# Kernel optimization log

Hardware: AMD Instinct MI355X
Metric: run time of the kernel (lower is better)

Reference implementation:

```python
import jax, jax.numpy as jnp
import numpy as np

N_NODES = 50000
N_EDGES = 600000
D_IN = 128
D_HID = 128
NUM_LAYERS = 4


def setup_inputs() -> dict:
    key = jax.random.key(0)
    ks = jax.random.split(key, 8)
    x = jax.random.normal(ks[0], (N_NODES, D_IN), dtype=jnp.float32)
    edge_index = jax.random.randint(ks[1], (2, N_EDGES), 0, N_NODES, dtype=jnp.int32)
    s = 0.05
    # first_conv: lin_rel (weight+bias) applied to aggregated neighbors, lin_root (no bias) applied to x
    W1 = jax.random.normal(ks[2], (D_IN, D_HID), dtype=jnp.float32) * s
    b1 = jnp.zeros((D_HID,), dtype=jnp.float32)
    R1 = jax.random.normal(ks[3], (D_IN, D_HID), dtype=jnp.float32) * s
    # shared conv used for layers 2..NUM_LAYERS
    W2 = jax.random.normal(ks[4], (D_HID, D_HID), dtype=jnp.float32) * s
    b2 = jnp.zeros((D_HID,), dtype=jnp.float32)
    R2 = jax.random.normal(ks[5], (D_HID, D_HID), dtype=jnp.float32) * s
    return {"x": x, "edge_index": edge_index, "W1": W1, "b1": b1, "R1": R1,
            "W2": W2, "b2": b2, "R2": R2}


def _graph_conv(x, src, dst, W, b, R, num_nodes):
    # gather source features, scatter-max into destinations (PyG GraphConv, aggr='max')
    agg = jax.ops.segment_max(x[src], dst, num_segments=num_nodes)  # [N, d]
    agg = jnp.where(jnp.isneginf(agg), 0.0, agg)  # isolated nodes -> 0 (PyG fill)
    return agg @ W + b + x @ R  # lin_rel(agg) + lin_root(x)


def reference(x, edge_index, W1, b1, R1, W2, b2, R2):
    src, dst = edge_index[0], edge_index[1]
    n = x.shape[0]
    h = jax.nn.relu(_graph_conv(x, src, dst, W1, b1, R1, n))
    for _ in range(NUM_LAYERS - 1):  # shared weights, per original module
        h = jax.nn.relu(_graph_conv(h, src, dst, W2, b2, R2, n))
    return h
```

## Files before the change

### kernel.cpp

```cpp
#include <hip/hip_runtime.h>
#include <math.h>

static constexpr int NNODES = 50000;
static constexpr int NEDGES = 600000;
static constexpr int D = 128;

typedef __attribute__((ext_vector_type(8))) short short8;
typedef __attribute__((ext_vector_type(4))) float f32x4;

static __device__ inline unsigned short f2bf_rne(float f) {
  unsigned u = __float_as_uint(f);
  unsigned r = (u + 0x7FFFu + ((u >> 16) & 1u)) >> 16;
  return (unsigned short)r;
}
static __device__ inline float bf2f(unsigned short s) {
  return __uint_as_float(((unsigned)s) << 16);
}


__global__ void count_kernel(const int* __restrict__ dst, int* __restrict__ cnt, int nE) {
  int i = blockIdx.x * blockDim.x + threadIdx.x;
  if (i < nE) atomicAdd(&cnt[dst[i]], 1);
}

__global__ void scan_kernel(const int* __restrict__ cnt, int* __restrict__ rs, int n) {
  __shared__ int wsum[16];
  __shared__ int s_carry;
  if (threadIdx.x == 0) s_carry = 0;
  __syncthreads();
  const int wid = threadIdx.x >> 6;
  const int lane = threadIdx.x & 63;
  for (int base = 0; base < n; base += 1024) {
    int i = base + (int)threadIdx.x;
    int v = (i < n) ? cnt[i] : 0;
    int incl = v;
#pragma unroll
    for (int off = 1; off < 64; off <<= 1) {
      int t = __shfl_up(incl, off);
      if (lane >= off) incl += t;
    }
    if (lane == 63) wsum[wid] = incl;
    __syncthreads();
    int woff = s_carry;
    for (int w = 0; w < wid; ++w) woff += wsum[w];
    if (i < n) rs[i] = woff + incl - v;
    __syncthreads();
    if (threadIdx.x == 1023) s_carry = woff + incl;
    __syncthreads();
  }
  if (threadIdx.x == 0) rs[n] = s_carry;
}

__global__ void fill_kernel(const int* __restrict__ src, const int* __restrict__ dst,
                            int* __restrict__ cursor, int* __restrict__ csr, int nE) {
  int i = blockIdx.x * blockDim.x + threadIdx.x;
  if (i < nE) {
    int d = dst[i];
    int p = atomicAdd(&cursor[d], 1);
    csr[p] = src[i];
  }
}

__global__ __launch_bounds__(256) void agg_kernel(const float* __restrict__ x,
    const int* __restrict__ rs, const int* __restrict__ csr,
    float* __restrict__ agg, int n) {
  int gw = (int)((blockIdx.x * blockDim.x + threadIdx.x) >> 6);
  int lane = threadIdx.x & 63;
  if (gw >= n) return;
  int beg = rs[gw], end = rs[gw + 1];
  const float2* xx = (const float2*)x;
  float2 acc;
  acc.x = -INFINITY; acc.y = -INFINITY;
  int j = beg;
  for (; j + 4 <= end; j += 4) {
    int s0 = csr[j], s1 = csr[j + 1], s2 = csr[j + 2], s3 = csr[j + 3];
    float2 v0 = xx[s0 * 64 + lane];
    float2 v1 = xx[s1 * 64 + lane];
    float2 v2 = xx[s2 * 64 + lane];
    float2 v3 = xx[s3 * 64 + lane];
    acc.x = fmaxf(fmaxf(fmaxf(v0.x, v1.x), fmaxf(v2.x, v3.x)), acc.x);
    acc.y = fmaxf(fmaxf(fmaxf(v0.y, v1.y), fmaxf(v2.y, v3.y)), acc.y);
  }
  for (; j < end; ++j) {
    int s = csr[j];
    float2 v = xx[s * 64 + lane];
    acc.x = fmaxf(acc.x, v.x);
    acc.y = fmaxf(acc.y, v.y);
  }
  if (beg == end) { acc.x = 0.f; acc.y = 0.f; }
  ((float2*)agg)[gw * 64 + lane] = acc;
}

__global__ void pack_kernel(const float* __restrict__ Wm,
                            unsigned short* __restrict__ hi,
                            unsigned short* __restrict__ lo) {
  int tid = blockIdx.x * blockDim.x + threadIdx.x;
  if (tid >= 2048) return;
  int jb = tid >> 8;
  int ks = (tid >> 6) & 3;
  int lane = tid & 63;
  int j = jb * 16 + (lane & 15);
  int k0 = ks * 32 + (lane >> 4) * 8;
#pragma unroll
  for (int e = 0; e < 8; ++e) {
    float v = Wm[(k0 + e) * D + j];
    unsigned short h = f2bf_rne(v);
    float rem = v - bf2f(h);
    unsigned short l = f2bf_rne(rem);
    hi[tid * 8 + e] = h;
    lo[tid * 8 + e] = l;
  }
}

__global__ __launch_bounds__(256) void gemm_mfma(
    const float* __restrict__ agg, const float* __restrict__ hin,
    const unsigned short* __restrict__ Whi, const unsigned short* __restrict__ Wlo,
    const unsigned short* __restrict__ Rhi, const unsigned short* __restrict__ Rlo,
    const float* __restrict__ bias, float* __restrict__ out, int nrows) {
  const int lane = threadIdx.x & 63;
  const int wv = threadIdx.x >> 6;
  const int m_lo = lane & 15;
  const int kgrp = lane >> 4;
  const int r_base = blockIdx.x * 128 + wv * 32;

  f32x4 acc[2][8];
#pragma unroll
  for (int g = 0; g < 2; ++g)
#pragma unroll
    for (int jb = 0; jb < 8; ++jb) acc[g][jb] = (f32x4)0.f;

  float bv[8];
#pragma unroll
  for (int jb = 0; jb < 8; ++jb) bv[jb] = bias[jb * 16 + m_lo];

  for (int ks = 0; ks < 4; ++ks) {
    short8 fa_hi[2], fa_lo[2], fh_hi[2], fh_lo[2];
#pragma unroll
    for (int g = 0; g < 2; ++g) {
      int row = r_base + g * 16 + m_lo;
      if (row >= nrows) row = nrows - 1;
      const float* ap = agg + (size_t)row * D + ks * 32 + kgrp * 8;
      const float* hp = hin + (size_t)row * D + ks * 32 + kgrp * 8;
      float av[8], hv[8];
      *(f32x4*)&av[0] = *(const f32x4*)(ap);
      *(f32x4*)&av[4] = *(const f32x4*)(ap + 4);
      *(f32x4*)&hv[0] = *(const f32x4*)(hp);
      *(f32x4*)&hv[4] = *(const f32x4*)(hp + 4);
#pragma unroll
      for (int e = 0; e < 8; ++e) {
        unsigned short h1 = f2bf_rne(av[e]);
        fa_hi[g][e] = (short)h1;
        fa_lo[g][e] = (short)f2bf_rne(av[e] - bf2f(h1));
        unsigned short h2 = f2bf_rne(hv[e]);
        fh_hi[g][e] = (short)h2;
        fh_lo[g][e] = (short)f2bf_rne(hv[e] - bf2f(h2));
      }
    }
#pragma unroll
    for (int jb = 0; jb < 8; ++jb) {
      const int pidx = ((jb * 4 + ks) * 64 + lane) * 8;
      short8 bwhi = *(const short8*)(Whi + pidx);
      short8 bwlo = *(const short8*)(Wlo + pidx);
      short8 brhi = *(const short8*)(Rhi + pidx);
      short8 brlo = *(const short8*)(Rlo + pidx);
#pragma unroll
      for (int g = 0; g < 2; ++g) {
        acc[g][jb] = __builtin_amdgcn_mfma_f32_16x16x32_bf16(fa_hi[g], bwhi, acc[g][jb], 0, 0, 0);
        acc[g][jb] = __builtin_amdgcn_mfma_f32_16x16x32_bf16(fa_lo[g], bwhi, acc[g][jb], 0, 0, 0);
        acc[g][jb] = __builtin_amdgcn_mfma_f32_16x16x32_bf16(fa_hi[g], bwlo, acc[g][jb], 0, 0, 0);
        acc[g][jb] = __builtin_amdgcn_mfma_f32_16x16x32_bf16(fh_hi[g], brhi, acc[g][jb], 0, 0, 0);
        acc[g][jb] = __builtin_amdgcn_mfma_f32_16x16x32_bf16(fh_lo[g], brhi, acc[g][jb], 0, 0, 0);
        acc[g][jb] = __builtin_amdgcn_mfma_f32_16x16x32_bf16(fh_hi[g], brlo, acc[g][jb], 0, 0, 0);
      }
    }
  }

#pragma unroll
  for (int g = 0; g < 2; ++g) {
#pragma unroll
    for (int jb = 0; jb < 8; ++jb) {
#pragma unroll
      for (int r = 0; r < 4; ++r) {
        int row = r_base + g * 16 + kgrp * 4 + r;
        if (row < nrows) {
          float v = acc[g][jb][r] + bv[jb];
          out[(size_t)row * D + jb * 16 + m_lo] = fmaxf(v, 0.f);
        }
      }
    }
  }
}


extern "C" void kernel_launch(void* const* d_in, const int* in_sizes, int n_in,
                              void* d_out, int out_size, void* d_ws, size_t ws_size,
                              hipStream_t stream) {
  const float* x  = (const float*)d_in[0];
  const int*   ei = (const int*)d_in[1];
  const float* W1 = (const float*)d_in[2];
  const float* b1 = (const float*)d_in[3];
  const float* R1 = (const float*)d_in[4];
  const float* W2 = (const float*)d_in[5];
  const float* b2 = (const float*)d_in[6];
  const float* R2 = (const float*)d_in[7];
  float* out = (float*)d_out;

  const int* src = ei;
  const int* dst = ei + NEDGES;

  char* ws = (char*)d_ws;
  size_t off = 0;
  auto alloc = [&](size_t bytes) -> void* {
    off = (off + 511) & ~(size_t)511;
    void* p = ws + off;
    off += bytes;
    return p;
  };
  float* aggbuf = (float*)alloc(sizeof(float) * (size_t)NNODES * D);
  float* hbuf   = (float*)alloc(sizeof(float) * (size_t)NNODES * D);
  int* cnt      = (int*)alloc(sizeof(int) * NNODES);
  int* rs       = (int*)alloc(sizeof(int) * (NNODES + 1));
  int* cursor   = (int*)alloc(sizeof(int) * NNODES);
  int* csr      = (int*)alloc(sizeof(int) * NEDGES);
  const int PACKN = 2048 * 8;
  unsigned short* w1hi = (unsigned short*)alloc(sizeof(short) * PACKN);
  unsigned short* w1lo = (unsigned short*)alloc(sizeof(short) * PACKN);
  unsigned short* r1hi = (unsigned short*)alloc(sizeof(short) * PACKN);
  unsigned short* r1lo = (unsigned short*)alloc(sizeof(short) * PACKN);
  unsigned short* w2hi = (unsigned short*)alloc(sizeof(short) * PACKN);
  unsigned short* w2lo = (unsigned short*)alloc(sizeof(short) * PACKN);
  unsigned short* r2hi = (unsigned short*)alloc(sizeof(short) * PACKN);
  unsigned short* r2lo = (unsigned short*)alloc(sizeof(short) * PACKN);

  pack_kernel<<<8, 256, 0, stream>>>(W1, w1hi, w1lo);
  pack_kernel<<<8, 256, 0, stream>>>(R1, r1hi, r1lo);
  pack_kernel<<<8, 256, 0, stream>>>(W2, w2hi, w2lo);
  pack_kernel<<<8, 256, 0, stream>>>(R2, r2hi, r2lo);

  hipMemsetAsync(cnt, 0, sizeof(int) * NNODES, stream);
  count_kernel<<<(NEDGES + 255) / 256, 256, 0, stream>>>(dst, cnt, NEDGES);
  scan_kernel<<<1, 1024, 0, stream>>>(cnt, rs, NNODES);
  hipMemcpyAsync(cursor, rs, sizeof(int) * NNODES, hipMemcpyDeviceToDevice, stream);
  fill_kernel<<<(NEDGES + 255) / 256, 256, 0, stream>>>(src, dst, cursor, csr, NEDGES);

  const int gemm_grid = (NNODES + 127) / 128;

  auto layer = [&](const float* hin,
                   const unsigned short* whi, const unsigned short* wlo,
                   const unsigned short* rhi, const unsigned short* rlo,
                   const float* b, float* hout) {
    agg_kernel<<<(NNODES + 3) / 4, 256, 0, stream>>>(hin, rs, csr, aggbuf, NNODES);
    gemm_mfma<<<gemm_grid, 256, 0, stream>>>(aggbuf, hin, whi, wlo, rhi, rlo, b, hout, NNODES);
  };

  layer(x,    w1hi, w1lo, r1hi, r1lo, b1, hbuf);
  layer(hbuf, w2hi, w2lo, r2hi, r2lo, b2, out);
  layer(out,  w2hi, w2lo, r2hi, r2lo, b2, hbuf);
  layer(hbuf, w2hi, w2lo, r2hi, r2lo, b2, out);
}
```

Baseline: 475.8 us.

## Parallelize CSR prefix scan, batch weight packing, deepen gather unroll

Replaces the single-block serial scan over node counts with a three-kernel multi-block scan (partial sums, root scan, apply) that also writes the cursor array, dropping the device-to-device copy. The four weight-pack launches are merged into one launch taking a struct of pointers. The max-aggregation gather loop issues eight independent row loads per iteration instead of four, to expose more memory-level parallelism. This adds two launches for the scan but removes a long serial single-block kernel. The root scan handles only up to 256 partial sums, which fits the 196 partitions here.

Measured after the change: 415.3 us. -12.7%, faster.

```diff
diff --git a/kernel.cpp b/kernel.cpp
--- a/kernel.cpp
+++ b/kernel.cpp
@@ -4,6 +4,7 @@
 static constexpr int NNODES = 50000;
 static constexpr int NEDGES = 600000;
 static constexpr int D = 128;
+static constexpr int NPART = (NNODES + 255) / 256;
 
 typedef __attribute__((ext_vector_type(8))) short short8;
 typedef __attribute__((ext_vector_type(4))) float f32x4;
@@ -23,32 +24,56 @@
   if (i < nE) atomicAdd(&cnt[dst[i]], 1);
 }
 
-__global__ void scan_kernel(const int* __restrict__ cnt, int* __restrict__ rs, int n) {
-  __shared__ int wsum[16];
-  __shared__ int s_carry;
-  if (threadIdx.x == 0) s_carry = 0;
+__global__ void scan_partial(const int* __restrict__ cnt, int* __restrict__ part, int n) {
+  int i = blockIdx.x * 256 + threadIdx.x;
+  int v = (i < n) ? cnt[i] : 0;
+#pragma unroll
+  for (int off = 32; off > 0; off >>= 1) v += __shfl_down(v, off);
+  __shared__ int ws[4];
+  int wid = threadIdx.x >> 6, lane = threadIdx.x & 63;
+  if (lane == 0) ws[wid] = v;
   __syncthreads();
-  const int wid = threadIdx.x >> 6;
-  const int lane = threadIdx.x & 63;
-  for (int base = 0; base < n; base += 1024) {
-    int i = base + (int)threadIdx.x;
-    int v = (i < n) ? cnt[i] : 0;
-    int incl = v;
-#pragma unroll
-    for (int off = 1; off < 64; off <<= 1) {
-      int t = __shfl_up(incl, off);
-      if (lane >= off) incl += t;
-    }
-    if (lane == 63) wsum[wid] = incl;
-    __syncthreads();
-    int woff = s_carry;
-    for (int w = 0; w < wid; ++w) woff += wsum[w];
-    if (i < n) rs[i] = woff + incl - v;
-    __syncthreads();
-    if (threadIdx.x == 1023) s_carry = woff + incl;
-    __syncthreads();
-  }
-  if (threadIdx.x == 0) rs[n] = s_carry;
+  if (threadIdx.x == 0) part[blockIdx.x] = ws[0] + ws[1] + ws[2] + ws[3];
+}
+
+__global__ void scan_root(const int* __restrict__ part, int* __restrict__ pscan,
+                          int* __restrict__ rs_last, int np) {
+  int i = threadIdx.x;
+  int v = (i < np) ? part[i] : 0;
+  int incl = v;
+  int lane = i & 63, wid = i >> 6;
+#pragma unroll
+  for (int off = 1; off < 64; off <<= 1) {
+    int t = __shfl_up(incl, off);
+    if (lane >= off) incl += t;
+  }
+  __shared__ int ws[4];
+  if (lane == 63) ws[wid] = incl;
+  __syncthreads();
+  int woff = 0;
+  for (int w = 0; w < wid; ++w) woff += ws[w];
+  if (i < np) pscan[i] = woff + incl - v;
+  if (i == 0) *rs_last = ws[0] + ws[1] + ws[2] + ws[3];
+}
+
+__global__ void scan_apply(const int* __restrict__ cnt, const int* __restrict__ pscan,
+                           int* __restrict__ rs, int* __restrict__ cursor, int n) {
+  int i = blockIdx.x * 256 + threadIdx.x;
+  int v = (i < n) ? cnt[i] : 0;
+  int incl = v;
+  int lane = threadIdx.x & 63, wid = threadIdx.x >> 6;
+#pragma unroll
+  for (int off = 1; off < 64; off <<= 1) {
+    int t = __shfl_up(incl, off);
+    if (lane >= off) incl += t;
+  }
+  __shared__ int ws[4];
+  if (lane == 63) ws[wid] = incl;
+  __syncthreads();
+  int woff = pscan[blockIdx.x];
+  for (int w = 0; w < wid; ++w) woff += ws[w];
+  int ex = woff + incl - v;
+  if (i < n) { rs[i] = ex; cursor[i] = ex; }
 }
 
 __global__ void fill_kernel(const int* __restrict__ src, const int* __restrict__ dst,
@@ -72,14 +97,25 @@
   float2 acc;
   acc.x = -INFINITY; acc.y = -INFINITY;
   int j = beg;
-  for (; j + 4 <= end; j += 4) {
-    int s0 = csr[j], s1 = csr[j + 1], s2 = csr[j + 2], s3 = csr[j + 3];
+  for (; j + 8 <= end; j += 8) {
+    int s[8];
+#pragma unroll
+    for (int u = 0; u < 8; ++u) s[u] = csr[j + u];
+    float2 v[8];
+#pragma unroll
+    for (int u = 0; u < 8; ++u) v[u] = xx[s[u] * 64 + lane];
+#pragma unroll
+    for (int u = 0; u < 8; ++u) {
+      acc.x = fmaxf(acc.x, v[u].x);
+      acc.y = fmaxf(acc.y, v[u].y);
+    }
+  }
+  for (; j + 2 <= end; j += 2) {
+    int s0 = csr[j], s1 = csr[j + 1];
     float2 v0 = xx[s0 * 64 + lane];
     float2 v1 = xx[s1 * 64 + lane];
-    float2 v2 = xx[s2 * 64 + lane];
-    float2 v3 = xx[s3 * 64 + lane];
-    acc.x = fmaxf(fmaxf(fmaxf(v0.x, v1.x), fmaxf(v2.x, v3.x)), acc.x);
-    acc.y = fmaxf(fmaxf(fmaxf(v0.y, v1.y), fmaxf(v2.y, v3.y)), acc.y);
+    acc.x = fmaxf(acc.x, fmaxf(v0.x, v1.x));
+    acc.y = fmaxf(acc.y, fmaxf(v0.y, v1.y));
   }
   for (; j < end; ++j) {
     int s = csr[j];
@@ -91,11 +127,18 @@
   ((float2*)agg)[gw * 64 + lane] = acc;
 }
 
-__global__ void pack_kernel(const float* __restrict__ Wm,
-                            unsigned short* __restrict__ hi,
-                            unsigned short* __restrict__ lo) {
-  int tid = blockIdx.x * blockDim.x + threadIdx.x;
-  if (tid >= 2048) return;
+struct PackArgs {
+  const float* src[4];
+  unsigned short* hi[4];
+  unsigned short* lo[4];
+};
+
+__global__ void pack_all(PackArgs pa) {
+  int mat = blockIdx.x >> 3;
+  int tid = (blockIdx.x & 7) * 256 + threadIdx.x;
+  const float* Wm = pa.src[mat];
+  unsigned short* hi = pa.hi[mat];
+  unsigned short* lo = pa.lo[mat];
   int jb = tid >> 8;
   int ks = (tid >> 6) & 3;
   int lane = tid & 63;
@@ -222,6 +265,8 @@
   int* rs       = (int*)alloc(sizeof(int) * (NNODES + 1));
   int* cursor   = (int*)alloc(sizeof(int) * NNODES);
   int* csr      = (int*)alloc(sizeof(int) * NEDGES);
+  int* part     = (int*)alloc(sizeof(int) * NPART);
+  int* pscan    = (int*)alloc(sizeof(int) * NPART);
   const int PACKN = 2048 * 8;
   unsigned short* w1hi = (unsigned short*)alloc(sizeof(short) * PACKN);
   unsigned short* w1lo = (unsigned short*)alloc(sizeof(short) * PACKN);
@@ -232,15 +277,18 @@
   unsigned short* r2hi = (unsigned short*)alloc(sizeof(short) * PACKN);
   unsigned short* r2lo = (unsigned short*)alloc(sizeof(short) * PACKN);
 
-  pack_kernel<<<8, 256, 0, stream>>>(W1, w1hi, w1lo);
-  pack_kernel<<<8, 256, 0, stream>>>(R1, r1hi, r1lo);
-  pack_kernel<<<8, 256, 0, stream>>>(W2, w2hi, w2lo);
-  pack_kernel<<<8, 256, 0, stream>>>(R2, r2hi, r2lo);
+  PackArgs pa;
+  pa.src[0] = W1; pa.hi[0] = w1hi; pa.lo[0] = w1lo;
+  pa.src[1] = R1; pa.hi[1] = r1hi; pa.lo[1] = r1lo;
+  pa.src[2] = W2; pa.hi[2] = w2hi; pa.lo[2] = w2lo;
+  pa.src[3] = R2; pa.hi[3] = r2hi; pa.lo[3] = r2lo;
+  pack_all<<<32, 256, 0, stream>>>(pa);
 
   hipMemsetAsync(cnt, 0, sizeof(int) * NNODES, stream);
   count_kernel<<<(NEDGES + 255) / 256, 256, 0, stream>>>(dst, cnt, NEDGES);
-  scan_kernel<<<1, 1024, 0, stream>>>(cnt, rs, NNODES);
-  hipMemcpyAsync(cursor, rs, sizeof(int) * NNODES, hipMemcpyDeviceToDevice, stream);
+  scan_partial<<<NPART, 256, 0, stream>>>(cnt, part, NNODES);
+  scan_root<<<1, 256, 0, stream>>>(part, pscan, &rs[NNODES], NPART);
+  scan_apply<<<NPART, 256, 0, stream>>>(cnt, pscan, rs, cursor, NNODES);
   fill_kernel<<<(NEDGES + 255) / 256, 256, 0, stream>>>(src, dst, cursor, csr, NEDGES);
 
   const int gemm_grid = (NNODES + 127) / 128;
```
